# Optimization experiments

Hardware: AMD Instinct MI355X
Metric: run time of the kernel (lower is better)

Reference implementation:

```python
import jax, jax.numpy as jnp
from jax import lax
import numpy as np

N_FEAT = 64
EMB = 128
HID = 2 * EMB  # 256
B, T = 256, 512


def _uniform(key, shape, bound):
    return jax.random.uniform(key, shape, jnp.float32, -bound, bound)


def setup_inputs() -> dict:
    key = jax.random.key(0)
    ks = jax.random.split(key, 9)
    x = jax.random.normal(ks[0], (B, T, N_FEAT), jnp.float32)
    b1 = 1.0 / np.sqrt(HID)
    b2 = 1.0 / np.sqrt(EMB)
    return {
        "x": x,
        "Wih1": _uniform(ks[1], (4 * HID, N_FEAT), b1),
        "Whh1": _uniform(ks[2], (4 * HID, HID), b1),
        "bih1": _uniform(ks[3], (4 * HID,), b1),
        "bhh1": _uniform(ks[4], (4 * HID,), b1),
        "Wih2": _uniform(ks[5], (4 * EMB, HID), b2),
        "Whh2": _uniform(ks[6], (4 * EMB, EMB), b2),
        "bih2": _uniform(ks[7], (4 * EMB,), b2),
        "bhh2": _uniform(ks[8], (4 * EMB,), b2),
    }


def lstm_layer(x, Wih, Whh, bih, bhh):
    """Single-layer batch_first LSTM, PyTorch gate order (i, f, g, o)."""
    Bb = x.shape[0]
    H = Whh.shape[1]
    # Precompute input contribution for all timesteps: [B, T, 4H]
    xg = jnp.einsum('bti,gi->btg', x, Wih) + bih + bhh

    def step(carry, g_t):
        h, c = carry
        gates = g_t + h @ Whh.T  # [B, 4H]
        i, f, g, o = jnp.split(gates, 4, axis=-1)
        i = jax.nn.sigmoid(i)
        f = jax.nn.sigmoid(f)
        g = jnp.tanh(g)
        o = jax.nn.sigmoid(o)
        c = f * c + i * g
        h = o * jnp.tanh(c)
        return (h, c), h

    h0 = jnp.zeros((Bb, H), x.dtype)
    (_, _), hs = lax.scan(step, (h0, h0), jnp.swapaxes(xg, 0, 1))  # hs: [T, B, H]
    return jnp.swapaxes(hs, 0, 1)


def reference(x, Wih1, Whh1, bih1, bhh1, Wih2, Whh2, bih2, bhh2):
    h1 = lstm_layer(x, Wih1, Whh1, bih1, bhh1)   # [B, T, 2E]
    h2 = lstm_layer(h1, Wih2, Whh2, bih2, bhh2)  # [B, T, E]
    return h2, h2[:, -1, :]
```

## Files before the change

### kernel.cpp

```cpp
#include <hip/hip_runtime.h>

typedef _Float16 half8 __attribute__((ext_vector_type(8)));
typedef float f32x4 __attribute__((ext_vector_type(4)));
typedef unsigned long long ull;

#define Bb 256
#define Tt 512
#define NF 64
#define H1u 256
#define H2u 128
#define NGRP 16
#define Bs 16
#define NBLK 64
#define NTHR 256

#define NF1 10
#define NF2 12
#define NT1 4
#define NT2 2

#define OFFB_WF1 0
#define SZB_WF1  (16*4*NF1*64*16)
#define OFFB_WF2 (OFFB_WF1+SZB_WF1)
#define SZB_WF2  (16*2*NF2*64*16)
#define OFFB_BF1 (OFFB_WF2+SZB_WF2)
#define SZB_BF1  (16*4*4*4*4)
#define OFFB_BF2 (OFFB_BF1+SZB_BF1)
#define SZB_BF2  (16*2*4*4*4)
#define OFFB_PAN (OFFB_BF2+SZB_BF2)
#define SZB_PAN  (2*16*48*16*16)
#define OFFB_CTR (OFFB_PAN+SZB_PAN)
#define SZB_CTR  (NGRP*64)

__device__ __forceinline__ float sigf(float x) {
    return 1.0f / (1.0f + __expf(-x));
}
__device__ __forceinline__ float tanhfast(float x) {
    return 2.0f / (1.0f + __expf(-2.0f * x)) - 1.0f;
}

__global__ __launch_bounds__(256) void prep4(
    const float* __restrict__ Wih1, const float* __restrict__ Whh1,
    const float* __restrict__ bih1, const float* __restrict__ bhh1,
    const float* __restrict__ Wih2, const float* __restrict__ Whh2,
    const float* __restrict__ bih2, const float* __restrict__ bhh2,
    char* __restrict__ wsb)
{
    _Float16* wf1 = (_Float16*)(wsb + OFFB_WF1);
    _Float16* wf2 = (_Float16*)(wsb + OFFB_WF2);
    float*    bf1 = (float*)(wsb + OFFB_BF1);
    float*    bf2 = (float*)(wsb + OFFB_BF2);
    const int stride = gridDim.x * blockDim.x;
    const int i0 = blockIdx.x * blockDim.x + threadIdx.x;

    for (int idx = i0; idx < 16*4*NF1*64; idx += stride) {
        const int lane = idx & 63;
        int q = idx >> 6;
        const int f = q % NF1;  q /= NF1;
        const int tt = q & 3;
        const int w  = q >> 2;
        const int r = lane & 15;
        const int unit = w*16 + tt*4 + (r >> 2);
        const int gate = r & 3;
        const int grow = gate * H1u + unit;
        _Float16* dst = wf1 + (size_t)idx * 8;
        #pragma unroll
        for (int e = 0; e < 8; ++e) {
            const int k = f*32 + (lane >> 4)*8 + e;
            const float v = (k < NF) ? Wih1[grow*NF + k]
                                     : Whh1[grow*H1u + (k - NF)];
            dst[e] = (_Float16)v;
        }
    }
    for (int idx = i0; idx < 16*2*NF2*64; idx += stride) {
        const int lane = idx & 63;
        int q = idx >> 6;
        const int f = q % NF2;  q /= NF2;
        const int tt = q & 1;
        const int w  = q >> 1;
        const int r = lane & 15;
        const int unit = w*8 + tt*4 + (r >> 2);
        const int gate = r & 3;
        const int grow = gate * H2u + unit;
        _Float16* dst = wf2 + (size_t)idx * 8;
        #pragma unroll
        for (int e = 0; e < 8; ++e) {
            const int k = f*32 + (lane >> 4)*8 + e;
            const float v = (k < H1u) ? Wih2[grow*H1u + k]
                                      : Whh2[grow*H2u + (k - H1u)];
            dst[e] = (_Float16)v;
        }
    }
    for (int idx = i0; idx < 16*4*4*4; idx += stride) {
        const int reg = idx & 3, lg = (idx >> 2) & 3;
        const int tt = (idx >> 4) & 3, w = idx >> 6;
        const int unit = w*16 + tt*4 + lg;
        const int grow = reg * H1u + unit;
        bf1[idx] = bih1[grow] + bhh1[grow];
    }
    for (int idx = i0; idx < 16*2*4*4; idx += stride) {
        const int reg = idx & 3, lg = (idx >> 2) & 3;
        const int tt = (idx >> 4) & 1, w = idx >> 5;
        const int unit = w*8 + tt*4 + lg;
        const int grow = reg * H2u + unit;
        bf2[idx] = bih2[grow] + bhh2[grow];
    }
}

__global__ __launch_bounds__(NTHR, 1) void lstm_v5(
    const float* __restrict__ x, const char* __restrict__ wsb,
    ull* pan, unsigned* ctrs, float* __restrict__ out)
{
    const int tid   = threadIdx.x;
    const int w     = tid >> 6;
    const int lane  = tid & 63;
    const int g     = lane >> 4;
    const int b     = lane & 15;
    const int grp   = blockIdx.x & 15;
    const int slice = blockIdx.x >> 4;
    const int W     = slice * 4 + w;
    const int b0    = grp * Bs;

    const _Float16* wf1g = (const _Float16*)(wsb + OFFB_WF1);
    const _Float16* wf2g = (const _Float16*)(wsb + OFFB_WF2);
    const float*    bf1g = (const float*)(wsb + OFFB_BF1);
    const float*    bf2g = (const float*)(wsb + OFFB_BF2);

    half8 wA1[NT1][NF1];
    half8 wA2[NT2][NF2];
    #pragma unroll
    for (int tt = 0; tt < NT1; ++tt)
        #pragma unroll
        for (int f = 0; f < NF1; ++f)
            wA1[tt][f] = *(const half8*)(wf1g + ((size_t)(((W*4 + tt)*NF1 + f) * 64 + lane)) * 8);
    #pragma unroll
    for (int tt = 0; tt < NT2; ++tt)
        #pragma unroll
        for (int f = 0; f < NF2; ++f)
            wA2[tt][f] = *(const half8*)(wf2g + ((size_t)(((W*2 + tt)*NF2 + f) * 64 + lane)) * 8);

    f32x4 bias1[NT1], bias2[NT2];
    #pragma unroll
    for (int tt = 0; tt < NT1; ++tt)
        bias1[tt] = *(const f32x4*)(bf1g + ((W*4 + tt)*4 + g) * 4);
    #pragma unroll
    for (int tt = 0; tt < NT2; ++tt)
        bias2[tt] = *(const f32x4*)(bf2g + ((W*2 + tt)*4 + g) * 4);

    float c1s[NT1] = {0.f, 0.f, 0.f, 0.f};
    float c2s[NT2] = {0.f, 0.f};

    unsigned* ctr = ctrs + grp * 16;
    unsigned short* pan16 = (unsigned short*)pan;

    for (int t = 0; t <= Tt; ++t) {
        const int parW1 = t & 1;
        const int parR1 = (t + 1) & 1;
        const int parW2 = (t + 1) & 1;
        const int parR2 = t & 1;

        const size_t base1 = (size_t)(parR1 * 16 + grp) * 1536;
        const size_t base2 = (size_t)(parR2 * 16 + grp) * 1536 + 1024;

        half8 bf1f[NF1];
        half8 bf2f[NF2];

        if (t < Tt) {
            #pragma unroll
            for (int f = 0; f < 2; ++f) {
                const float* xp = x + (((size_t)(b0 + b)) * Tt + t) * NF + f * 32 + g * 8;
                const float4 lo = *(const float4*)xp;
                const float4 hi = *(const float4*)(xp + 4);
                half8 v;
                v[0] = (_Float16)lo.x; v[1] = (_Float16)lo.y;
                v[2] = (_Float16)lo.z; v[3] = (_Float16)lo.w;
                v[4] = (_Float16)hi.x; v[5] = (_Float16)hi.y;
                v[6] = (_Float16)hi.z; v[7] = (_Float16)hi.w;
                bf1f[f] = v;
            }
            #pragma unroll
            for (int i = 0; i < 8; ++i) {
                const size_t a = base1 + (size_t)(4*i + g) * 32 + b * 2;
                union { ull q[2]; half8 h; } u;
                u.q[0] = __hip_atomic_load(pan + a,     __ATOMIC_RELAXED, __HIP_MEMORY_SCOPE_AGENT);
                u.q[1] = __hip_atomic_load(pan + a + 1, __ATOMIC_RELAXED, __HIP_MEMORY_SCOPE_AGENT);
                bf1f[2 + i] = u.h;
            }
        }
        if (t >= 1) {
            if (t < Tt) {
                #pragma unroll
                for (int f = 0; f < 8; ++f) bf2f[f] = bf1f[2 + f];
            } else {
                #pragma unroll
                for (int f = 0; f < 8; ++f) {
                    const size_t a = base1 + (size_t)(4*f + g) * 32 + b * 2;
                    union { ull q[2]; half8 h; } u;
                    u.q[0] = __hip_atomic_load(pan + a,     __ATOMIC_RELAXED, __HIP_MEMORY_SCOPE_AGENT);
                    u.q[1] = __hip_atomic_load(pan + a + 1, __ATOMIC_RELAXED, __HIP_MEMORY_SCOPE_AGENT);
                    bf2f[f] = u.h;
                }
            }
            #pragma unroll
            for (int f = 0; f < 4; ++f) {
                const size_t a = base2 + (size_t)(4*f + g) * 32 + b * 2;
                union { ull q[2]; half8 h; } u;
                u.q[0] = __hip_atomic_load(pan + a,     __ATOMIC_RELAXED, __HIP_MEMORY_SCOPE_AGENT);
                u.q[1] = __hip_atomic_load(pan + a + 1, __ATOMIC_RELAXED, __HIP_MEMORY_SCOPE_AGENT);
                bf2f[8 + f] = u.h;
            }
        }

        if (t < Tt) {
            f32x4 acc[NT1] = {};
            #pragma unroll
            for (int f = 0; f < NF1; ++f)
                #pragma unroll
                for (int tt = 0; tt < NT1; ++tt)
                    acc[tt] = __builtin_amdgcn_mfma_f32_16x16x32_f16(wA1[tt][f], bf1f[f], acc[tt], 0, 0, 0);
            #pragma unroll
            for (int tt = 0; tt < NT1; ++tt) {
                const float iv = sigf(acc[tt][0] + bias1[tt][0]);
                const float fv = sigf(acc[tt][1] + bias1[tt][1]);
                const float gv = tanhfast(acc[tt][2] + bias1[tt][2]);
                const float ov = sigf(acc[tt][3] + bias1[tt][3]);
                const float c = fmaf(fv, c1s[tt], iv * gv);
                c1s[tt] = c;
                const float h = ov * tanhfast(c);
                const int u = W * 16 + tt * 4 + g;
                union { _Float16 f; unsigned short s; } hc;
                hc.f = (_Float16)h;
                const size_t si = ((size_t)(parW1 * 16 + grp) * 48 + (u >> 3)) * 128 + b * 8 + (u & 7);
                __hip_atomic_store(pan16 + si, hc.s, __ATOMIC_RELAXED, __HIP_MEMORY_SCOPE_AGENT);
            }
        }
        if (t >= 1) {
            const int s = t - 1;
            f32x4 acc[NT2] = {};
            #pragma unroll
            for (int f = 0; f < NF2; ++f)
                #pragma unroll
                for (int tt = 0; tt < NT2; ++tt)
                    acc[tt] = __builtin_amdgcn_mfma_f32_16x16x32_f16(wA2[tt][f], bf2f[f], acc[tt], 0, 0, 0);
            #pragma unroll
            for (int tt = 0; tt < NT2; ++tt) {
                const float iv = sigf(acc[tt][0] + bias2[tt][0]);
                const float fv = sigf(acc[tt][1] + bias2[tt][1]);
                const float gv = tanhfast(acc[tt][2] + bias2[tt][2]);
                const float ov = sigf(acc[tt][3] + bias2[tt][3]);
                const float c = fmaf(fv, c2s[tt], iv * gv);
                c2s[tt] = c;
                const float h = ov * tanhfast(c);
                const int u2 = W * 8 + tt * 4 + g;
                union { _Float16 f; unsigned short s; } hc;
                hc.f = (_Float16)h;
                const size_t si = ((size_t)(parW2 * 16 + grp) * 48 + 32 + (u2 >> 3)) * 128 + b * 8 + (u2 & 7);
                __hip_atomic_store(pan16 + si, hc.s, __ATOMIC_RELAXED, __HIP_MEMORY_SCOPE_AGENT);
                out[((size_t)(b0 + b) * Tt + s) * H2u + u2] = h;
                if (s == Tt - 1)
                    out[(size_t)Bb * Tt * H2u + (size_t)(b0 + b) * H2u + u2] = h;
            }
        }
        if (t < Tt) {
            __syncthreads();
            if (tid == 0) {
                __hip_atomic_fetch_add(ctr, 1u, __ATOMIC_RELAXED, __HIP_MEMORY_SCOPE_AGENT);
                const unsigned tgt = 4u * (unsigned)(t + 1);
                while (__hip_atomic_load(ctr, __ATOMIC_RELAXED, __HIP_MEMORY_SCOPE_AGENT) < tgt)
                    __builtin_amdgcn_s_sleep(2);
            }
            __syncthreads();
        }
    }
}

extern "C" void kernel_launch(void* const* d_in, const int* in_sizes, int n_in,
                              void* d_out, int out_size, void* d_ws, size_t ws_size,
                              hipStream_t stream) {
    const float* x    = (const float*)d_in[0];
    const float* Wih1 = (const float*)d_in[1];
    const float* Whh1 = (const float*)d_in[2];
    const float* bih1 = (const float*)d_in[3];
    const float* bhh1 = (const float*)d_in[4];
    const float* Wih2 = (const float*)d_in[5];
    const float* Whh2 = (const float*)d_in[6];
    const float* bih2 = (const float*)d_in[7];
    const float* bhh2 = (const float*)d_in[8];
    char*  wsb = (char*)d_ws;
    float* out = (float*)d_out;

    prep4<<<256, 256, 0, stream>>>(Wih1, Whh1, bih1, bhh1,
                                   Wih2, Whh2, bih2, bhh2, wsb);
    hipMemsetAsync((void*)(wsb + OFFB_PAN), 0, SZB_PAN + SZB_CTR, stream);
    lstm_v5<<<NBLK, NTHR, 0, stream>>>(
        x, wsb, (ull*)(wsb + OFFB_PAN), (unsigned*)(wsb + OFFB_CTR), out);
}
```

Baseline: 2.019 ms.

## Replace block-level counter barrier with per-wave step flags and LDS-staged coalesced exchange

```diff
diff --git a/kernel.cpp b/kernel.cpp
--- a/kernel.cpp
+++ b/kernel.cpp
@@ -3,6 +3,12 @@
 typedef _Float16 half8 __attribute__((ext_vector_type(8)));
 typedef float f32x4 __attribute__((ext_vector_type(4)));
 typedef unsigned long long ull;
+
+typedef ull      __attribute__((may_alias)) ull_a;
+typedef unsigned __attribute__((may_alias)) u32_a;
+typedef float4   __attribute__((may_alias)) float4_a;
+
+#define LGKM_BAR() asm volatile("s_waitcnt lgkmcnt(0)" ::: "memory")
 
 #define Bb 256
 #define Tt 512
@@ -27,10 +33,12 @@
 #define SZB_BF1  (16*4*4*4*4)
 #define OFFB_BF2 (OFFB_BF1+SZB_BF1)
 #define SZB_BF2  (16*2*4*4*4)
-#define OFFB_PAN (OFFB_BF2+SZB_BF2)
-#define SZB_PAN  (2*16*48*16*16)
-#define OFFB_CTR (OFFB_PAN+SZB_PAN)
-#define SZB_CTR  (NGRP*64)
+#define OFFB_PH1 (OFFB_BF2+SZB_BF2)
+#define SZB_PH1  (2*16*8192)
+#define OFFB_PH2 (OFFB_PH1+SZB_PH1)
+#define SZB_PH2  (2*16*4096)
+#define OFFB_STM (OFFB_PH2+SZB_PH2)
+#define SZB_STM  (16*256)
 
 __device__ __forceinline__ float sigf(float x) {
     return 1.0f / (1.0f + __expf(-x));
@@ -107,10 +115,28 @@
     }
 }
 
-__global__ __launch_bounds__(NTHR, 1) void lstm_v5(
-    const float* __restrict__ x, const char* __restrict__ wsb,
-    ull* pan, unsigned* ctrs, float* __restrict__ out)
+__device__ __forceinline__ void load_x_frags(half8* xf, const float* __restrict__ x,
+                                             int b0, int b, int g, int t)
 {
+    #pragma unroll
+    for (int f = 0; f < 2; ++f) {
+        const float* xp = x + (((size_t)(b0 + b)) * Tt + t) * NF + f * 32 + g * 8;
+        const float4 lo = *(const float4*)xp;
+        const float4 hi = *(const float4*)(xp + 4);
+        half8 v;
+        v[0] = (_Float16)lo.x; v[1] = (_Float16)lo.y;
+        v[2] = (_Float16)lo.z; v[3] = (_Float16)lo.w;
+        v[4] = (_Float16)hi.x; v[5] = (_Float16)hi.y;
+        v[6] = (_Float16)hi.z; v[7] = (_Float16)hi.w;
+        xf[f] = v;
+    }
+}
+
+__global__ __launch_bounds__(NTHR, 1) void lstm_v7(
+    const float* __restrict__ x, char* wsb, float* __restrict__ out)
+{
+    __shared__ char ldsraw[4 * 2048];
+
     const int tid   = threadIdx.x;
     const int w     = tid >> 6;
     const int lane  = tid & 63;
@@ -125,6 +151,15 @@
     const _Float16* wf2g = (const _Float16*)(wsb + OFFB_WF2);
     const float*    bf1g = (const float*)(wsb + OFFB_BF1);
     const float*    bf2g = (const float*)(wsb + OFFB_BF2);
+    ull*            ph1  = (ull*)(wsb + OFFB_PH1);
+    ull*            ph2  = (ull*)(wsb + OFFB_PH2);
+    unsigned*       pu2  = (unsigned*)(wsb + OFFB_PH2);
+    unsigned*       stm  = (unsigned*)(wsb + OFFB_STM) + grp * 64;
+
+    char* myl = ldsraw + w * 2048;
+    _Float16* l_h1 = (_Float16*)(myl);
+    _Float16* l_h2 = (_Float16*)(myl + 512);
+    float*    l_o  = (float*)(myl + 1024);
 
     half8 wA1[NT1][NF1];
     half8 wA2[NT2][NF2];
@@ -150,74 +185,25 @@
     float c1s[NT1] = {0.f, 0.f, 0.f, 0.f};
     float c2s[NT2] = {0.f, 0.f};
 
-    unsigned* ctr = ctrs + grp * 16;
-    unsigned short* pan16 = (unsigned short*)pan;
+    half8 hz = {};
+    half8 hf[8]  = {hz, hz, hz, hz, hz, hz, hz, hz};
+    half8 h2f[4] = {hz, hz, hz, hz};
+    half8 xf[2];
+    load_x_frags(xf, x, b0, b, g, 0);
 
     for (int t = 0; t <= Tt; ++t) {
-        const int parW1 = t & 1;
-        const int parR1 = (t + 1) & 1;
-        const int parW2 = (t + 1) & 1;
-        const int parR2 = t & 1;
-
-        const size_t base1 = (size_t)(parR1 * 16 + grp) * 1536;
-        const size_t base2 = (size_t)(parR2 * 16 + grp) * 1536 + 1024;
-
-        half8 bf1f[NF1];
-        half8 bf2f[NF2];
-
-        if (t < Tt) {
-            #pragma unroll
-            for (int f = 0; f < 2; ++f) {
-                const float* xp = x + (((size_t)(b0 + b)) * Tt + t) * NF + f * 32 + g * 8;
-                const float4 lo = *(const float4*)xp;
-                const float4 hi = *(const float4*)(xp + 4);
-                half8 v;
-                v[0] = (_Float16)lo.x; v[1] = (_Float16)lo.y;
-                v[2] = (_Float16)lo.z; v[3] = (_Float16)lo.w;
-                v[4] = (_Float16)hi.x; v[5] = (_Float16)hi.y;
-                v[6] = (_Float16)hi.z; v[7] = (_Float16)hi.w;
-                bf1f[f] = v;
-            }
-            #pragma unroll
-            for (int i = 0; i < 8; ++i) {
-                const size_t a = base1 + (size_t)(4*i + g) * 32 + b * 2;
-                union { ull q[2]; half8 h; } u;
-                u.q[0] = __hip_atomic_load(pan + a,     __ATOMIC_RELAXED, __HIP_MEMORY_SCOPE_AGENT);
-                u.q[1] = __hip_atomic_load(pan + a + 1, __ATOMIC_RELAXED, __HIP_MEMORY_SCOPE_AGENT);
-                bf1f[2 + i] = u.h;
-            }
-        }
-        if (t >= 1) {
-            if (t < Tt) {
-                #pragma unroll
-                for (int f = 0; f < 8; ++f) bf2f[f] = bf1f[2 + f];
-            } else {
-                #pragma unroll
-                for (int f = 0; f < 8; ++f) {
-                    const size_t a = base1 + (size_t)(4*f + g) * 32 + b * 2;
-                    union { ull q[2]; half8 h; } u;
-                    u.q[0] = __hip_atomic_load(pan + a,     __ATOMIC_RELAXED, __HIP_MEMORY_SCOPE_AGENT);
-                    u.q[1] = __hip_atomic_load(pan + a + 1, __ATOMIC_RELAXED, __HIP_MEMORY_SCOPE_AGENT);
-                    bf2f[f] = u.h;
-                }
-            }
-            #pragma unroll
-            for (int f = 0; f < 4; ++f) {
-                const size_t a = base2 + (size_t)(4*f + g) * 32 + b * 2;
-                union { ull q[2]; half8 h; } u;
-                u.q[0] = __hip_atomic_load(pan + a,     __ATOMIC_RELAXED, __HIP_MEMORY_SCOPE_AGENT);
-                u.q[1] = __hip_atomic_load(pan + a + 1, __ATOMIC_RELAXED, __HIP_MEMORY_SCOPE_AGENT);
-                bf2f[8 + f] = u.h;
-            }
-        }
-
         if (t < Tt) {
             f32x4 acc[NT1] = {};
             #pragma unroll
-            for (int f = 0; f < NF1; ++f)
+            for (int tt = 0; tt < NT1; ++tt) {
+                acc[tt] = __builtin_amdgcn_mfma_f32_16x16x32_f16(wA1[tt][0], xf[0], acc[tt], 0, 0, 0);
+                acc[tt] = __builtin_amdgcn_mfma_f32_16x16x32_f16(wA1[tt][1], xf[1], acc[tt], 0, 0, 0);
+            }
+            #pragma unroll
+            for (int f = 0; f < 8; ++f)
                 #pragma unroll
                 for (int tt = 0; tt < NT1; ++tt)
-                    acc[tt] = __builtin_amdgcn_mfma_f32_16x16x32_f16(wA1[tt][f], bf1f[f], acc[tt], 0, 0, 0);
+                    acc[tt] = __builtin_amdgcn_mfma_f32_16x16x32_f16(wA1[tt][2 + f], hf[f], acc[tt], 0, 0, 0);
             #pragma unroll
             for (int tt = 0; tt < NT1; ++tt) {
                 const float iv = sigf(acc[tt][0] + bias1[tt][0]);
@@ -227,21 +213,28 @@
                 const float c = fmaf(fv, c1s[tt], iv * gv);
                 c1s[tt] = c;
                 const float h = ov * tanhfast(c);
-                const int u = W * 16 + tt * 4 + g;
-                union { _Float16 f; unsigned short s; } hc;
-                hc.f = (_Float16)h;
-                const size_t si = ((size_t)(parW1 * 16 + grp) * 48 + (u >> 3)) * 128 + b * 8 + (u & 7);
-                __hip_atomic_store(pan16 + si, hc.s, __ATOMIC_RELAXED, __HIP_MEMORY_SCOPE_AGENT);
+                const int ul = tt * 4 + g;
+                l_h1[((ul >> 3) * 16 + b) * 8 + (ul & 7)] = (_Float16)h;
+            }
+            LGKM_BAR();
+            {
+                const ull v = *(const ull_a*)(l_h1 + lane * 4);
+                const size_t di = ((size_t)((t & 1) * 16 + grp)) * 1024 + W * 64 + lane;
+                __hip_atomic_store(ph1 + di, v, __ATOMIC_RELAXED, __HIP_MEMORY_SCOPE_AGENT);
             }
         }
         if (t >= 1) {
-            const int s = t - 1;
             f32x4 acc[NT2] = {};
             #pragma unroll
-            for (int f = 0; f < NF2; ++f)
+            for (int f = 0; f < 8; ++f)
                 #pragma unroll
                 for (int tt = 0; tt < NT2; ++tt)
-                    acc[tt] = __builtin_amdgcn_mfma_f32_16x16x32_f16(wA2[tt][f], bf2f[f], acc[tt], 0, 0, 0);
+                    acc[tt] = __builtin_amdgcn_mfma_f32_16x16x32_f16(wA2[tt][f], hf[f], acc[tt], 0, 0, 0);
+            #pragma unroll
+            for (int f = 0; f < 4; ++f)
+                #pragma unroll
+                for (int tt = 0; tt < NT2; ++tt)
+                    acc[tt] = __builtin_amdgcn_mfma_f32_16x16x32_f16(wA2[tt][8 + f], h2f[f], acc[tt], 0, 0, 0);
             #pragma unroll
             for (int tt = 0; tt < NT2; ++tt) {
                 const float iv = sigf(acc[tt][0] + bias2[tt][0]);
@@ -251,25 +244,63 @@
                 const float c = fmaf(fv, c2s[tt], iv * gv);
                 c2s[tt] = c;
                 const float h = ov * tanhfast(c);
-                const int u2 = W * 8 + tt * 4 + g;
-                union { _Float16 f; unsigned short s; } hc;
-                hc.f = (_Float16)h;
-                const size_t si = ((size_t)(parW2 * 16 + grp) * 48 + 32 + (u2 >> 3)) * 128 + b * 8 + (u2 & 7);
-                __hip_atomic_store(pan16 + si, hc.s, __ATOMIC_RELAXED, __HIP_MEMORY_SCOPE_AGENT);
-                out[((size_t)(b0 + b) * Tt + s) * H2u + u2] = h;
-                if (s == Tt - 1)
-                    out[(size_t)Bb * Tt * H2u + (size_t)(b0 + b) * H2u + u2] = h;
+                const int ul = tt * 4 + g;
+                if (t < Tt) l_h2[b * 8 + ul] = (_Float16)h;
+                l_o[b * 8 + ul] = h;
+            }
+            LGKM_BAR();
+            if (t < Tt) {
+                const unsigned v = *(const u32_a*)((const _Float16*)l_h2 + lane * 2);
+                const size_t di = ((size_t)(((t + 1) & 1) * 16 + grp)) * 1024 + W * 64 + lane;
+                __hip_atomic_store(pu2 + di, v, __ATOMIC_RELAXED, __HIP_MEMORY_SCOPE_AGENT);
             }
         }
         if (t < Tt) {
-            __syncthreads();
-            if (tid == 0) {
-                __hip_atomic_fetch_add(ctr, 1u, __ATOMIC_RELAXED, __HIP_MEMORY_SCOPE_AGENT);
-                const unsigned tgt = 4u * (unsigned)(t + 1);
-                while (__hip_atomic_load(ctr, __ATOMIC_RELAXED, __HIP_MEMORY_SCOPE_AGENT) < tgt)
-                    __builtin_amdgcn_s_sleep(2);
-            }
-            __syncthreads();
+            asm volatile("s_waitcnt vmcnt(0)" ::: "memory");
+            if (lane == 0)
+                __hip_atomic_store(&stm[W], (unsigned)(t + 1),
+                                   __ATOMIC_RELAXED, __HIP_MEMORY_SCOPE_AGENT);
+        }
+        if (t >= 1 && lane < 32) {
+            const int s_ = t - 1;
+            const int bb = lane >> 1, q = lane & 1;
+            const float4 ov = *(const float4_a*)(l_o + bb * 8 + q * 4);
+            *(float4*)&out[((size_t)(b0 + bb) * Tt + s_) * H2u + W * 8 + q * 4] = ov;
+            if (s_ == Tt - 1)
+                *(float4*)&out[(size_t)Bb * Tt * H2u + (size_t)(b0 + bb) * H2u + W * 8 + q * 4] = ov;
+        }
+        if (t + 1 < Tt) load_x_frags(xf, x, b0, b, g, t + 1);
+        if (t < Tt) {
+            const int si = lane & 31;
+            const unsigned need = (si < 16) ? (unsigned)(t + 1) : (unsigned)t;
+            const unsigned* sp = stm + si;
+            for (;;) {
+                const unsigned v = __hip_atomic_load(sp, __ATOMIC_RELAXED, __HIP_MEMORY_SCOPE_AGENT);
+                if (__all((int)(v >= need))) break;
+                __builtin_amdgcn_s_sleep(1);
+            }
+            const size_t base1 = ((size_t)((t & 1) * 16 + grp)) * 1024;
+            #pragma unroll
+            for (int f = 0; f < 8; ++f) {
+                const size_t a = base1 + (size_t)(4 * f + g) * 32 + b * 2;
+                union { ull q[2]; half8 h; } u;
+                u.q[0] = __hip_atomic_load(ph1 + a,     __ATOMIC_RELAXED, __HIP_MEMORY_SCOPE_AGENT);
+                u.q[1] = __hip_atomic_load(ph1 + a + 1, __ATOMIC_RELAXED, __HIP_MEMORY_SCOPE_AGENT);
+                hf[f] = u.h;
+            }
+            const size_t base2 = ((size_t)(((t + 1) & 1) * 16 + grp)) * 512;
+            #pragma unroll
+            for (int f = 0; f < 4; ++f) {
+                const size_t a = base2 + (size_t)(4 * f + g) * 32 + b * 2;
+                union { ull q[2]; half8 h; } u;
+                u.q[0] = __hip_atomic_load(ph2 + a,     __ATOMIC_RELAXED, __HIP_MEMORY_SCOPE_AGENT);
+                u.q[1] = __hip_atomic_load(ph2 + a + 1, __ATOMIC_RELAXED, __HIP_MEMORY_SCOPE_AGENT);
+                h2f[f] = u.h;
+            }
+            asm volatile("s_waitcnt vmcnt(0)" ::: "memory");
+            if (lane == 0)
+                __hip_atomic_store(&stm[16 + W], (unsigned)(t + 1),
+                                   __ATOMIC_RELAXED, __HIP_MEMORY_SCOPE_AGENT);
         }
     }
 }
@@ -291,7 +322,6 @@
 
     prep4<<<256, 256, 0, stream>>>(Wih1, Whh1, bih1, bhh1,
                                    Wih2, Whh2, bih2, bhh2, wsb);
-    hipMemsetAsync((void*)(wsb + OFFB_PAN), 0, SZB_PAN + SZB_CTR, stream);
-    lstm_v5<<<NBLK, NTHR, 0, stream>>>(
-        x, wsb, (ull*)(wsb + OFFB_PAN), (unsigned*)(wsb + OFFB_CTR), out);
-}
+    hipMemsetAsync((void*)(wsb + OFFB_PH1), 0, SZB_PH1 + SZB_PH2 + SZB_STM, stream);
+    lstm_v7<<<NBLK, NTHR, 0, stream>>>(x, wsb, out);
+}
```

After: 2.061 ms. +2.1%, slower.
